# Kernel optimization log

Hardware: AMD Instinct MI355X
Metric: run time of the kernel (lower is better)

Reference implementation:

```python
import jax, jax.numpy as jnp
import numpy as np

N_PROP = 2048
N_CLS = 81  # background + 80 foreground classes
IMG_W, IMG_H = 1333.0, 800.0
SCORE_THRESH = 0.05
NMS_THRESH = 0.5
DET_PER_IMG = 100
BBOX_CLIP = float(np.log(1000.0 / 16.0))
TO_REMOVE = 1.0


def setup_inputs() -> dict:
    key = jax.random.key(0)
    k1, k2, k3, k4, k5, k6 = jax.random.split(key, 6)
    class_logits = jax.random.normal(k1, (N_PROP, N_CLS), jnp.float32)
    box_regression = jax.random.normal(k2, (N_PROP, N_CLS * 4), jnp.float32)
    # valid xyxy proposals inside the image
    x1 = jax.random.uniform(k3, (N_PROP,), jnp.float32, 0.0, IMG_W * 0.7)
    y1 = jax.random.uniform(k4, (N_PROP,), jnp.float32, 0.0, IMG_H * 0.7)
    w = jax.random.uniform(k5, (N_PROP,), jnp.float32, 16.0, IMG_W * 0.3)
    h = jax.random.uniform(k6, (N_PROP,), jnp.float32, 16.0, IMG_H * 0.3)
    proposals = jnp.stack([x1, y1, x1 + w, y1 + h], axis=-1)
    return {"class_logits": class_logits, "box_regression": box_regression, "proposals": proposals}


def decode_boxes(reg, props):
    # BoxCoder.decode with weights (10,10,5,5); reg: [N, C*4] -> [N, C, 4]
    widths = props[:, 2] - props[:, 0] + TO_REMOVE
    heights = props[:, 3] - props[:, 1] + TO_REMOVE
    ctr_x = props[:, 0] + 0.5 * widths
    ctr_y = props[:, 1] + 0.5 * heights
    r = reg.reshape(reg.shape[0], -1, 4)
    dx = r[..., 0] / 10.0
    dy = r[..., 1] / 10.0
    dw = jnp.minimum(r[..., 2] / 5.0, BBOX_CLIP)
    dh = jnp.minimum(r[..., 3] / 5.0, BBOX_CLIP)
    pcx = dx * widths[:, None] + ctr_x[:, None]
    pcy = dy * heights[:, None] + ctr_y[:, None]
    pw = jnp.exp(dw) * widths[:, None]
    ph = jnp.exp(dh) * heights[:, None]
    return jnp.stack([pcx - 0.5 * pw, pcy - 0.5 * ph,
                      pcx + 0.5 * pw - TO_REMOVE, pcy + 0.5 * ph - TO_REMOVE], axis=-1)


def pairwise_iou(b):
    # b: [N,4] xyxy -> [N,N] IoU with +1 pixel convention
    area = (b[:, 2] - b[:, 0] + TO_REMOVE) * (b[:, 3] - b[:, 1] + TO_REMOVE)
    lt = jnp.maximum(b[:, None, :2], b[None, :, :2])
    rb = jnp.minimum(b[:, None, 2:], b[None, :, 2:])
    wh = jnp.clip(rb - lt + TO_REMOVE, 0.0)
    inter = wh[..., 0] * wh[..., 1]
    return inter / (area[:, None] + area[None, :] - inter)


def nms_keep(boxes, scores, valid, thresh):
    # returns boolean keep mask (fixed shape) equivalent to greedy NMS on valid boxes
    n = scores.shape[0]
    order = jnp.argsort(-scores)
    b = boxes[order]
    v = valid[order]
    iou = pairwise_iou(b)  # [N,N]
    idx = jnp.arange(n)

    def step(suppressed, inp):
        row, vi, i = inp
        keep_i = vi & jnp.logical_not(suppressed[i])
        suppressed = suppressed | (keep_i & (row > thresh) & (idx > i))
        return suppressed, keep_i

    _, keep_sorted = jax.lax.scan(step, jnp.zeros(n, bool), (iou, v, idx))
    return jnp.zeros(n, bool).at[order].set(keep_sorted)


def _forward(class_logits, box_regression, proposals):
    probs = jax.nn.softmax(class_logits, axis=-1)          # [N, C]
    boxes = decode_boxes(box_regression, proposals)        # [N, C, 4]
    # clip_to_image (remove_empty=False)
    boxes = jnp.stack([jnp.clip(boxes[..., 0], 0.0, IMG_W - TO_REMOVE),
                       jnp.clip(boxes[..., 1], 0.0, IMG_H - TO_REMOVE),
                       jnp.clip(boxes[..., 2], 0.0, IMG_W - TO_REMOVE),
                       jnp.clip(boxes[..., 3], 0.0, IMG_H - TO_REMOVE)], axis=-1)
    # drop background class 0; class-major layout [C-1, N, ...]
    boxes_c = jnp.transpose(boxes[:, 1:, :], (1, 0, 2))    # [C-1, N, 4]
    scores_c = probs[:, 1:].T                              # [C-1, N]
    valid = scores_c > SCORE_THRESH
    keep = jax.vmap(nms_keep, in_axes=(0, 0, 0, None))(boxes_c, scores_c, valid, NMS_THRESH)
    masked = jnp.where(keep, scores_c, -1.0)               # invalid -> below any prob
    flat_scores = masked.reshape(-1)                       # [(C-1)*N]
    _, top_idx = jax.lax.top_k(flat_scores, DET_PER_IMG)
    out_scores = flat_scores[top_idx]
    out_boxes = boxes_c.reshape(-1, 4)[top_idx]
    out_labels = top_idx // N_PROP + 1                     # class labels in [1, C-1]
    return out_boxes, out_scores, out_labels


def reference(class_logits, box_regression, proposals):
    return _forward(class_logits, box_regression, proposals)
```

## Files before the change

### kernel.cpp

```cpp
#include <hip/hip_runtime.h>
#include <math.h>

#define NPROP 2048
#define NCLS 81
#define NFG 80
#define NBLK 80
#define CAP 512
#define TOPC 100
#define NB 1152
#define BMIN 0x7A99


#define LDS_FENCE() do { __builtin_amdgcn_wave_barrier(); \
    asm volatile("s_waitcnt lgkmcnt(0)" ::: "memory");     \
    __builtin_amdgcn_wave_barrier(); } while (0)

__device__ __forceinline__ void decode_clip(const float* __restrict__ props,
                                            const float* __restrict__ reg,
                                            int p, int cls, float out[4]) {
    float px1 = props[p * 4 + 0], py1 = props[p * 4 + 1];
    float px2 = props[p * 4 + 2], py2 = props[p * 4 + 3];
    float w = px2 - px1 + 1.0f;
    float h = py2 - py1 + 1.0f;
    float cx = px1 + 0.5f * w;
    float cy = py1 + 0.5f * h;
    const float* r = reg + (size_t)p * (NCLS * 4) + cls * 4;
    float dx = r[0] / 10.0f;
    float dy = r[1] / 10.0f;
    float dw = fminf(r[2] / 5.0f, 4.135166556742356f);
    float dh = fminf(r[3] / 5.0f, 4.135166556742356f);
    float pcx = dx * w + cx;
    float pcy = dy * h + cy;
    float pw = expf(dw) * w;
    float ph = expf(dh) * h;
    float x1 = pcx - 0.5f * pw;
    float y1 = pcy - 0.5f * ph;
    float x2 = pcx + 0.5f * pw - 1.0f;
    float y2 = pcy + 0.5f * ph - 1.0f;
    out[0] = fminf(fmaxf(x1, 0.0f), 1332.0f);
    out[1] = fminf(fmaxf(y1, 0.0f), 799.0f);
    out[2] = fminf(fmaxf(x2, 0.0f), 1332.0f);
    out[3] = fminf(fmaxf(y2, 0.0f), 799.0f);
}

__global__ __launch_bounds__(256) void softmax_scatter(const float* __restrict__ logits,
                                                       unsigned long long* __restrict__ cand,
                                                       int* __restrict__ bar) {
    if (blockIdx.x == 0 && threadIdx.x == 0) *bar = 0;
    int gw = (blockIdx.x * blockDim.x + threadIdx.x) >> 6;
    int lane = threadIdx.x & 63;
    if (gw >= NPROP) return;
    const float* row = logits + (size_t)gw * NCLS;
    float a = row[lane];
    bool hasb = (lane + 64) < NCLS;
    float b = hasb ? row[lane + 64] : -INFINITY;
    float m = fmaxf(a, b);
    #pragma unroll
    for (int s = 32; s; s >>= 1) m = fmaxf(m, __shfl_xor(m, s));
    float ea = expf(a - m);
    float eb = hasb ? expf(b - m) : 0.0f;
    float sum = ea + eb;
    #pragma unroll
    for (int s = 32; s; s >>= 1) sum += __shfl_xor(sum, s);
    float pa = ea / sum;
    float pb = eb / sum;
    unsigned int np = (unsigned int)(~gw);
    if (lane != 0) {
        cand[(size_t)(lane - 1) * NPROP + gw] = (pa > 0.05f)
            ? (((unsigned long long)__float_as_uint(pa) << 32) | np) : 0ULL;
    }
    if (hasb) {
        cand[(size_t)(lane + 63) * NPROP + gw] = (pb > 0.05f)
            ? (((unsigned long long)__float_as_uint(pb) << 32) | np) : 0ULL;
    }
}

__global__ __launch_bounds__(256) void nms_topk(const unsigned long long* __restrict__ cand,
                                                const float* __restrict__ props,
                                                const float* __restrict__ reg,
                                                int* __restrict__ bar,
                                                int* __restrict__ scnt,
                                                unsigned long long* __restrict__ surv,
                                                float* __restrict__ out) {
    const int c = blockIdx.x;
    const int tid = threadIdx.x;
    const int lane = tid & 63;
    const int bw = tid >> 6;
    __shared__ unsigned long long keys[CAP];
    __shared__ float4 bxs[CAP];
    __shared__ unsigned int hist[NB];
    __shared__ unsigned long long comp[1024];
    __shared__ int s_n[NFG];
    __shared__ int sB;
    __shared__ int compN;

    if (bw == 0) {
        const unsigned long long* col = cand + (size_t)c * NPROP;
        int base = 0;
        for (int p0 = 0; p0 < NPROP; p0 += 64) {
            unsigned long long key = col[p0 + lane];
            bool keep = key != 0ULL;
            unsigned long long mask = __ballot(keep);
            if (keep) {
                int pos = base + __popcll(mask & ((1ULL << lane) - 1ULL));
                if (pos < CAP) keys[pos] = key;
            }
            base += __popcll(mask);
        }
        int M = base > CAP ? CAP : base;
        int nsurv = 0;
        if (M > 0) {
            int S = 64;
            while (S < M) S <<= 1;
            for (int i = lane; i < S; i += 64)
                if (i >= M) keys[i] = 0ULL;
            LDS_FENCE();

            for (int k = 2; k <= S; k <<= 1) {
                for (int j = k >> 1; j > 0; j >>= 1) {
                    for (int i = lane; i < S; i += 64) {
                        int l = i ^ j;
                        if (l > i) {
                            unsigned long long A = keys[i], B = keys[l];
                            bool dir = ((i & k) == 0);
                            if ((A < B) == dir) { keys[i] = B; keys[l] = A; }
                        }
                    }
                    LDS_FENCE();
                }
            }

            float4 myb[8];
            #pragma unroll
            for (int ns = 0; ns < 8; ++ns) {
                int idx = lane + ns * 64;
                if (idx < M) {
                    unsigned long long key = keys[idx];
                    int p = (int)(~(unsigned int)key);
                    float b4[4];
                    decode_clip(props, reg, p, c + 1, b4);
                    float4 f = make_float4(b4[0], b4[1], b4[2], b4[3]);
                    myb[ns] = f;
                    bxs[idx] = f;
                }
            }
            LDS_FENCE();

            unsigned int my_sup = 0u;
            for (int i = 0; i < M; ++i) {
                int owner = i & 63, slot = i >> 6;
                unsigned int os = __shfl(my_sup, owner);
                if ((os >> slot) & 1u) continue;
                float4 bi = bxs[i];
                float ai = (bi.z - bi.x + 1.0f) * (bi.w - bi.y + 1.0f);
                #pragma unroll
                for (int ns = 0; ns < 8; ++ns) {
                    int j = lane + ns * 64;
                    if (j < M && j > i) {
                        float4 bj = myb[ns];
                        float aj = (bj.z - bj.x + 1.0f) * (bj.w - bj.y + 1.0f);
                        float ltx = fmaxf(bi.x, bj.x), lty = fmaxf(bi.y, bj.y);
                        float rbx = fminf(bi.z, bj.z), rby = fminf(bi.w, bj.w);
                        float iw = fmaxf(rbx - ltx + 1.0f, 0.0f);
                        float ih = fmaxf(rby - lty + 1.0f, 0.0f);
                        float inter = iw * ih;
                        float iou = inter / (ai + aj - inter);
                        if (iou > 0.5f) my_sup |= (1u << ns);
                    }
                }
            }

            #pragma unroll
            for (int ns = 0; ns < 8; ++ns) {
                if (ns * 64 >= M) break;
                int j = lane + ns * 64;
                bool keep = (j < M) && !((my_sup >> ns) & 1u);
                unsigned long long mask = __ballot(keep);
                if (keep) {
                    int pos = nsurv + __popcll(mask & ((1ULL << lane) - 1ULL));
                    if (pos < TOPC) {
                        unsigned long long key = keys[j];
                        int p = (int)(~(unsigned int)key);
                        unsigned int flat = (unsigned int)(c * NPROP + p);
                        surv[c * TOPC + pos] =
                            (key & 0xFFFFFFFF00000000ULL) | (unsigned int)(~flat);
                    }
                }
                nsurv += __popcll(mask);
            }
        }
        if (lane == 0) scnt[c] = nsurv;
    }

    __syncthreads();
    if (tid == 0) {
        __threadfence();
        atomicAdd(bar, 1);
    }
    if (blockIdx.x != 0) return;
    if (tid == 0) {
        int guard = 0;
        while (__hip_atomic_load(bar, __ATOMIC_ACQUIRE,
                                 __HIP_MEMORY_SCOPE_AGENT) < NBLK) {
            if (++guard > (1 << 24)) break;
        }
    }
    __syncthreads();
    __threadfence();

    for (int i = tid; i < NB; i += 256) hist[i] = 0u;
    if (tid < NFG) {
        int k = scnt[tid];
        s_n[tid] = (k > TOPC) ? TOPC : k;
    }
    if (tid == 0) compN = 0;
    __syncthreads();

    for (int idx = tid; idx < NFG * TOPC; idx += 256) {
        int cc = idx / TOPC, i = idx - cc * TOPC;
        if (i < s_n[cc]) {
            unsigned long long key = surv[idx];
            int b = (int)(((unsigned int)(key >> 32)) >> 15) - BMIN;
            b = b < 0 ? 0 : (b >= NB ? NB - 1 : b);
            atomicAdd(&hist[b], 1u);
        }
    }
    __syncthreads();

    if (tid < 64) {
        int running = 0, Bstar = 0;
        bool found = false;
        for (int chunk = NB - 64; chunk >= 0; chunk -= 64) {
            int b = chunk + 63 - tid;
            int s = (int)hist[b];
            #pragma unroll
            for (int d = 1; d < 64; d <<= 1) {
                int o = __shfl_up(s, d);
                if (tid >= d) s += o;
            }
            int cum = running + s;
            unsigned long long m = __ballot(cum >= TOPC);
            if (m != 0ULL) {
                int l = (int)__ffsll((unsigned long long)m) - 1;
                Bstar = chunk + 63 - l;
                found = true;
                break;
            }
            running += __shfl(s, 63);
        }
        if (!found) Bstar = 0;
        if (tid == 0) sB = Bstar;
    }
    __syncthreads();
    int Bstar = sB;

    for (int idx = tid; idx < NFG * TOPC; idx += 256) {
        int cc = idx / TOPC, i = idx - cc * TOPC;
        if (i < s_n[cc]) {
            unsigned long long key = surv[idx];
            int b = (int)(((unsigned int)(key >> 32)) >> 15) - BMIN;
            b = b < 0 ? 0 : (b >= NB ? NB - 1 : b);
            if (b >= Bstar) {
                int pos = atomicAdd(&compN, 1);
                if (pos < 1024) comp[pos] = key;
            }
        }
    }
    __syncthreads();
    int K = compN;
    if (K > 1024) K = 1024;
    int P = 128;
    while (P < K) P <<= 1;
    for (int i = K + tid; i < P; i += 256) comp[i] = 0ULL;
    __syncthreads();

    if (tid < 64) {
        for (int k = 2; k <= P; k <<= 1) {
            for (int j = k >> 1; j > 0; j >>= 1) {
                for (int i = tid; i < P; i += 64) {
                    int l = i ^ j;
                    if (l > i) {
                        unsigned long long A = comp[i], B = comp[l];
                        bool dir = ((i & k) == 0);
                        if ((A < B) == dir) { comp[i] = B; comp[l] = A; }
                    }
                }
                LDS_FENCE();
            }
        }
    }
    __syncthreads();

    if (tid < TOPC) {
        unsigned long long key = comp[tid];
        float score;
        int flat;
        if (key == 0ULL) {
            score = -1.0f;
            flat = tid;
        } else {
            score = __uint_as_float((unsigned int)(key >> 32));
            flat = (int)(~(unsigned int)key);
        }
        int cc = flat >> 11;
        int p = flat & (NPROP - 1);
        float b4[4];
        decode_clip(props, reg, p, cc + 1, b4);
        out[tid * 4 + 0] = b4[0];
        out[tid * 4 + 1] = b4[1];
        out[tid * 4 + 2] = b4[2];
        out[tid * 4 + 3] = b4[3];
        out[400 + tid] = score;
        out[500 + tid] = (float)(cc + 1);
    }
}

extern "C" void kernel_launch(void* const* d_in, const int* in_sizes, int n_in,
                              void* d_out, int out_size, void* d_ws, size_t ws_size,
                              hipStream_t stream) {
    const float* logits = (const float*)d_in[0];
    const float* reg    = (const float*)d_in[1];
    const float* props  = (const float*)d_in[2];
    float* out = (float*)d_out;

    int* bar  = (int*)d_ws;
    int* scnt = (int*)((char*)d_ws + 64);
    unsigned long long* surv = (unsigned long long*)((char*)d_ws + 384);
    unsigned long long* cand = (unsigned long long*)((char*)d_ws + 65536);

    hipLaunchKernelGGL(softmax_scatter, dim3((NPROP * 64) / 256), dim3(256), 0, stream,
                       logits, cand, bar);
    hipLaunchKernelGGL(nms_topk, dim3(NBLK), dim3(256), 0, stream,
                       cand, props, reg, bar, scnt, surv, out);
}
```

Measured before the change: 139.1 us.

## Split fused NMS/top-k kernel into separate launches, drop global spin barrier

Replaces the single kernel, which had a last-block atomic spin barrier, with two kernels: a 64-thread per-class NMS kernel and a single-block top-k kernel, so ordering comes from the stream instead of a global barrier. The NMS kernel also preloads all 32 candidate chunks into registers before compaction to overlap global loads. It removes the spin-wait and the three idle waves per block, but adds an extra kernel launch and more register pressure from the 32-element preload.

```diff
diff --git a/kernel.cpp b/kernel.cpp
--- a/kernel.cpp
+++ b/kernel.cpp
@@ -4,7 +4,6 @@
 #define NPROP 2048
 #define NCLS 81
 #define NFG 80
-#define NBLK 80
 #define CAP 512
 #define TOPC 100
 #define NB 1152
@@ -44,9 +43,7 @@
 }
 
 __global__ __launch_bounds__(256) void softmax_scatter(const float* __restrict__ logits,
-                                                       unsigned long long* __restrict__ cand,
-                                                       int* __restrict__ bar) {
-    if (blockIdx.x == 0 && threadIdx.x == 0) *bar = 0;
+                                                       unsigned long long* __restrict__ cand) {
     int gw = (blockIdx.x * blockDim.x + threadIdx.x) >> 6;
     int lane = threadIdx.x & 63;
     if (gw >= NPROP) return;
@@ -75,138 +72,128 @@
     }
 }
 
-__global__ __launch_bounds__(256) void nms_topk(const unsigned long long* __restrict__ cand,
-                                                const float* __restrict__ props,
-                                                const float* __restrict__ reg,
-                                                int* __restrict__ bar,
-                                                int* __restrict__ scnt,
-                                                unsigned long long* __restrict__ surv,
-                                                float* __restrict__ out) {
+__global__ __launch_bounds__(64) void nms_kernel(const unsigned long long* __restrict__ cand,
+                                                 const float* __restrict__ props,
+                                                 const float* __restrict__ reg,
+                                                 int* __restrict__ scnt,
+                                                 unsigned long long* __restrict__ surv) {
     const int c = blockIdx.x;
-    const int tid = threadIdx.x;
-    const int lane = tid & 63;
-    const int bw = tid >> 6;
+    const int lane = threadIdx.x;
     __shared__ unsigned long long keys[CAP];
     __shared__ float4 bxs[CAP];
+
+    const unsigned long long* col = cand + (size_t)c * NPROP;
+    unsigned long long v[32];
+    #pragma unroll
+    for (int t = 0; t < 32; ++t) v[t] = col[t * 64 + lane];
+
+    int base = 0;
+    #pragma unroll
+    for (int t = 0; t < 32; ++t) {
+        bool keep = v[t] != 0ULL;
+        unsigned long long mask = __ballot(keep);
+        if (keep) {
+            int pos = base + __popcll(mask & ((1ULL << lane) - 1ULL));
+            if (pos < CAP) keys[pos] = v[t];
+        }
+        base += __popcll(mask);
+    }
+    int M = base > CAP ? CAP : base;
+    int nsurv = 0;
+    if (M > 0) {
+        int S = 64;
+        while (S < M) S <<= 1;
+        for (int i = lane; i < S; i += 64)
+            if (i >= M) keys[i] = 0ULL;
+        LDS_FENCE();
+
+        for (int k = 2; k <= S; k <<= 1) {
+            for (int j = k >> 1; j > 0; j >>= 1) {
+                for (int i = lane; i < S; i += 64) {
+                    int l = i ^ j;
+                    if (l > i) {
+                        unsigned long long A = keys[i], B = keys[l];
+                        bool dir = ((i & k) == 0);
+                        if ((A < B) == dir) { keys[i] = B; keys[l] = A; }
+                    }
+                }
+                LDS_FENCE();
+            }
+        }
+
+        float4 myb[8];
+        #pragma unroll
+        for (int ns = 0; ns < 8; ++ns) {
+            int idx = lane + ns * 64;
+            if (idx < M) {
+                unsigned long long key = keys[idx];
+                int p = (int)(~(unsigned int)key);
+                float b4[4];
+                decode_clip(props, reg, p, c + 1, b4);
+                float4 f = make_float4(b4[0], b4[1], b4[2], b4[3]);
+                myb[ns] = f;
+                bxs[idx] = f;
+            }
+        }
+        LDS_FENCE();
+
+        unsigned int my_sup = 0u;
+        for (int i = 0; i < M; ++i) {
+            int owner = i & 63, slot = i >> 6;
+            unsigned int os = __shfl(my_sup, owner);
+            if ((os >> slot) & 1u) continue;
+            float4 bi = bxs[i];
+            float ai = (bi.z - bi.x + 1.0f) * (bi.w - bi.y + 1.0f);
+            #pragma unroll
+            for (int ns = 0; ns < 8; ++ns) {
+                int j = lane + ns * 64;
+                if (j < M && j > i) {
+                    float4 bj = myb[ns];
+                    float aj = (bj.z - bj.x + 1.0f) * (bj.w - bj.y + 1.0f);
+                    float ltx = fmaxf(bi.x, bj.x), lty = fmaxf(bi.y, bj.y);
+                    float rbx = fminf(bi.z, bj.z), rby = fminf(bi.w, bj.w);
+                    float iw = fmaxf(rbx - ltx + 1.0f, 0.0f);
+                    float ih = fmaxf(rby - lty + 1.0f, 0.0f);
+                    float inter = iw * ih;
+                    float iou = inter / (ai + aj - inter);
+                    if (iou > 0.5f) my_sup |= (1u << ns);
+                }
+            }
+        }
+
+        #pragma unroll
+        for (int ns = 0; ns < 8; ++ns) {
+            if (ns * 64 >= M) break;
+            int j = lane + ns * 64;
+            bool keep = (j < M) && !((my_sup >> ns) & 1u);
+            unsigned long long mask = __ballot(keep);
+            if (keep) {
+                int pos = nsurv + __popcll(mask & ((1ULL << lane) - 1ULL));
+                if (pos < TOPC) {
+                    unsigned long long key = keys[j];
+                    int p = (int)(~(unsigned int)key);
+                    unsigned int flat = (unsigned int)(c * NPROP + p);
+                    surv[c * TOPC + pos] =
+                        (key & 0xFFFFFFFF00000000ULL) | (unsigned int)(~flat);
+                }
+            }
+            nsurv += __popcll(mask);
+        }
+    }
+    if (lane == 0) scnt[c] = nsurv;
+}
+
+__global__ __launch_bounds__(256) void topk_kernel(const int* __restrict__ scnt,
+                                                   const unsigned long long* __restrict__ surv,
+                                                   const float* __restrict__ props,
+                                                   const float* __restrict__ reg,
+                                                   float* __restrict__ out) {
     __shared__ unsigned int hist[NB];
     __shared__ unsigned long long comp[1024];
     __shared__ int s_n[NFG];
     __shared__ int sB;
     __shared__ int compN;
-
-    if (bw == 0) {
-        const unsigned long long* col = cand + (size_t)c * NPROP;
-        int base = 0;
-        for (int p0 = 0; p0 < NPROP; p0 += 64) {
-            unsigned long long key = col[p0 + lane];
-            bool keep = key != 0ULL;
-            unsigned long long mask = __ballot(keep);
-            if (keep) {
-                int pos = base + __popcll(mask & ((1ULL << lane) - 1ULL));
-                if (pos < CAP) keys[pos] = key;
-            }
-            base += __popcll(mask);
-        }
-        int M = base > CAP ? CAP : base;
-        int nsurv = 0;
-        if (M > 0) {
-            int S = 64;
-            while (S < M) S <<= 1;
-            for (int i = lane; i < S; i += 64)
-                if (i >= M) keys[i] = 0ULL;
-            LDS_FENCE();
-
-            for (int k = 2; k <= S; k <<= 1) {
-                for (int j = k >> 1; j > 0; j >>= 1) {
-                    for (int i = lane; i < S; i += 64) {
-                        int l = i ^ j;
-                        if (l > i) {
-                            unsigned long long A = keys[i], B = keys[l];
-                            bool dir = ((i & k) == 0);
-                            if ((A < B) == dir) { keys[i] = B; keys[l] = A; }
-                        }
-                    }
-                    LDS_FENCE();
-                }
-            }
-
-            float4 myb[8];
-            #pragma unroll
-            for (int ns = 0; ns < 8; ++ns) {
-                int idx = lane + ns * 64;
-                if (idx < M) {
-                    unsigned long long key = keys[idx];
-                    int p = (int)(~(unsigned int)key);
-                    float b4[4];
-                    decode_clip(props, reg, p, c + 1, b4);
-                    float4 f = make_float4(b4[0], b4[1], b4[2], b4[3]);
-                    myb[ns] = f;
-                    bxs[idx] = f;
-                }
-            }
-            LDS_FENCE();
-
-            unsigned int my_sup = 0u;
-            for (int i = 0; i < M; ++i) {
-                int owner = i & 63, slot = i >> 6;
-                unsigned int os = __shfl(my_sup, owner);
-                if ((os >> slot) & 1u) continue;
-                float4 bi = bxs[i];
-                float ai = (bi.z - bi.x + 1.0f) * (bi.w - bi.y + 1.0f);
-                #pragma unroll
-                for (int ns = 0; ns < 8; ++ns) {
-                    int j = lane + ns * 64;
-                    if (j < M && j > i) {
-                        float4 bj = myb[ns];
-                        float aj = (bj.z - bj.x + 1.0f) * (bj.w - bj.y + 1.0f);
-                        float ltx = fmaxf(bi.x, bj.x), lty = fmaxf(bi.y, bj.y);
-                        float rbx = fminf(bi.z, bj.z), rby = fminf(bi.w, bj.w);
-                        float iw = fmaxf(rbx - ltx + 1.0f, 0.0f);
-                        float ih = fmaxf(rby - lty + 1.0f, 0.0f);
-                        float inter = iw * ih;
-                        float iou = inter / (ai + aj - inter);
-                        if (iou > 0.5f) my_sup |= (1u << ns);
-                    }
-                }
-            }
-
-            #pragma unroll
-            for (int ns = 0; ns < 8; ++ns) {
-                if (ns * 64 >= M) break;
-                int j = lane + ns * 64;
-                bool keep = (j < M) && !((my_sup >> ns) & 1u);
-                unsigned long long mask = __ballot(keep);
-                if (keep) {
-                    int pos = nsurv + __popcll(mask & ((1ULL << lane) - 1ULL));
-                    if (pos < TOPC) {
-                        unsigned long long key = keys[j];
-                        int p = (int)(~(unsigned int)key);
-                        unsigned int flat = (unsigned int)(c * NPROP + p);
-                        surv[c * TOPC + pos] =
-                            (key & 0xFFFFFFFF00000000ULL) | (unsigned int)(~flat);
-                    }
-                }
-                nsurv += __popcll(mask);
-            }
-        }
-        if (lane == 0) scnt[c] = nsurv;
-    }
-
-    __syncthreads();
-    if (tid == 0) {
-        __threadfence();
-        atomicAdd(bar, 1);
-    }
-    if (blockIdx.x != 0) return;
-    if (tid == 0) {
-        int guard = 0;
-        while (__hip_atomic_load(bar, __ATOMIC_ACQUIRE,
-                                 __HIP_MEMORY_SCOPE_AGENT) < NBLK) {
-            if (++guard > (1 << 24)) break;
-        }
-    }
-    __syncthreads();
-    __threadfence();
+    const int tid = threadIdx.x;
 
     for (int i = tid; i < NB; i += 256) hist[i] = 0u;
     if (tid < NFG) {
@@ -323,13 +310,14 @@
     const float* props  = (const float*)d_in[2];
     float* out = (float*)d_out;
 
-    int* bar  = (int*)d_ws;
-    int* scnt = (int*)((char*)d_ws + 64);
+    int* scnt = (int*)d_ws;
     unsigned long long* surv = (unsigned long long*)((char*)d_ws + 384);
     unsigned long long* cand = (unsigned long long*)((char*)d_ws + 65536);
 
     hipLaunchKernelGGL(softmax_scatter, dim3((NPROP * 64) / 256), dim3(256), 0, stream,
-                       logits, cand, bar);
-    hipLaunchKernelGGL(nms_topk, dim3(NBLK), dim3(256), 0, stream,
-                       cand, props, reg, bar, scnt, surv, out);
-}
+                       logits, cand);
+    hipLaunchKernelGGL(nms_kernel, dim3(NFG), dim3(64), 0, stream,
+                       cand, props, reg, scnt, surv);
+    hipLaunchKernelGGL(topk_kernel, dim3(1), dim3(256), 0, stream,
+                       scnt, surv, props, reg, out);
+}
```

New measurement: 131.1 us. 1.06x faster.
